# Kernel optimization log

Measured on AMD Instinct MI355X. Metric: run time of the kernel, lower is better.

Reference implementation:

```python
import jax, jax.numpy as jnp
import numpy as np

H = 768
NHEADS = 2
MAX_REL = 96  # module's max_rel_enc; static here (positive count >> 96 for these inputs)


def _ln(x, g, b, eps=1e-5):
    m = jnp.mean(x, axis=-1, keepdims=True)
    v = jnp.var(x, axis=-1, keepdims=True)
    return (x - m) * jax.lax.rsqrt(v + eps) * g + b


def _mha(q, k, v, in_w, in_b, out_w, out_b, key_pad):
    # q [B,Lq,H], k/v [B,Lk,H], key_pad [B,Lk] bool (True = masked key)
    d = q.shape[-1]
    dh = d // NHEADS
    wq, wk, wv = jnp.split(in_w, 3, axis=0)
    bq, bk, bv = jnp.split(in_b, 3)
    qh = (q @ wq.T + bq).reshape(q.shape[0], q.shape[1], NHEADS, dh)
    kh = (k @ wk.T + bk).reshape(k.shape[0], k.shape[1], NHEADS, dh)
    vh = (v @ wv.T + bv).reshape(v.shape[0], v.shape[1], NHEADS, dh)
    scores = jnp.einsum('bqhd,bkhd->bhqk', qh, kh) / np.float32(np.sqrt(dh))
    scores = jnp.where(key_pad[:, None, None, :], jnp.float32(-1e9), scores)
    attn = jax.nn.softmax(scores, axis=-1)
    out = jnp.einsum('bhqk,bkhd->bqhd', attn, vh).reshape(q.shape)
    return out @ out_w.T + out_b


def _forward(hidden_states, logits_prev, block_mask, W_rel, b_rel,
             enc_in_w, enc_in_b, enc_out_w, enc_out_b,
             enc_l1_w, enc_l1_b, enc_l2_w, enc_l2_b,
             enc_ln1_g, enc_ln1_b, enc_ln2_g, enc_ln2_b,
             dec_in_w, dec_in_b, dec_out_w, dec_out_b,
             dec_l1_w, dec_l1_b, dec_l2_w, dec_l2_b,
             dec_ln1_g, dec_ln1_b, dec_ln2_g, dec_ln2_b,
             fc_w, fc_b):
    B, N, Hd = hidden_states.shape
    # rel_layer(cat([h_i, h_j])) == h_i @ Wa.T + h_j @ Wb.T + b  (avoids [B,N,N,2H] intermediate)
    Wa = W_rel[:, :Hd]
    Wb = W_rel[:, Hd:]
    A = hidden_states @ Wa.T   # [B,N,H]
    C = hidden_states @ Wb.T   # [B,N,H]
    feat_pair = (A[:, :, None, :] + C[:, None, :, :] + b_rel).reshape(B, N * N, Hd)

    bm = block_mask.astype(jnp.float32)
    pair_mask = (bm[:, :, None] * bm[:, None, :]).reshape(B, N * N)
    score = jax.nn.sigmoid(logits_prev).reshape(B, N * N)
    neg = (score < 0.5).astype(jnp.float32)
    neg = 1.0 - (1.0 - neg) * pair_mask           # 1 = negative-or-invalid pair
    neg = jax.lax.stop_gradient(neg)              # matches score_prev.detach_()

    # dynamic top-k gather of positive pairs (static MAX_REL here)
    idx = jnp.argsort(neg, axis=1)[:, :MAX_REL]                     # positives (neg==0) first
    enc_pad = jnp.take_along_axis(neg, idx, axis=1) > 0.5           # [B,MAX_REL]
    enc_pad = enc_pad.at[:, 0].set(False)
    feat_now = feat_pair * (1.0 - neg)[:, :, None]
    pos_pairs = jnp.take_along_axis(feat_now, idx[:, :, None], axis=1)  # [B,MAX_REL,H]

    # 1-layer transformer encoder (post-norm, ReLU, d_ff = H)
    x = pos_pairs
    x = _ln(x + _mha(x, x, x, enc_in_w, enc_in_b, enc_out_w, enc_out_b, enc_pad),
            enc_ln1_g, enc_ln1_b)
    ff = jax.nn.relu(x @ enc_l1_w.T + enc_l1_b) @ enc_l2_w.T + enc_l2_b
    patterns = _ln(x + ff, enc_ln2_g, enc_ln2_b)

    # 1-layer decoder with self_attn=False: cross-attn + FFN, post-norm
    t = feat_pair
    t = _ln(t + _mha(t, patterns, patterns, dec_in_w, dec_in_b, dec_out_w, dec_out_b, enc_pad),
            dec_ln1_g, dec_ln1_b)
    ff = jax.nn.relu(t @ dec_l1_w.T + dec_l1_b) @ dec_l2_w.T + dec_l2_b
    t = _ln(t + ff, dec_ln2_g, dec_ln2_b)

    refined = t.reshape(B, N, N, Hd)
    return (refined @ fc_w.T + fc_b)[..., 0]    # [B,N,N]


def setup_inputs() -> dict:
    key = jax.random.key(0)
    ks = jax.random.split(key, 24)
    B, N = 4, 128
    p = lambda k, s: jax.random.normal(k, s, jnp.float32) * 0.02
    return {
        'hidden_states': jax.random.normal(ks[0], (B, N, H), jnp.float32),
        'logits_prev': jax.random.normal(ks[1], (B, N, N), jnp.float32),
        'block_mask': jax.random.randint(ks[2], (B, N), 0, 2),
        'W_rel': p(ks[3], (H, 2 * H)), 'b_rel': p(ks[4], (H,)),
        'enc_in_w': p(ks[5], (3 * H, H)), 'enc_in_b': p(ks[6], (3 * H,)),
        'enc_out_w': p(ks[7], (H, H)), 'enc_out_b': p(ks[8], (H,)),
        'enc_l1_w': p(ks[9], (H, H)), 'enc_l1_b': p(ks[10], (H,)),
        'enc_l2_w': p(ks[11], (H, H)), 'enc_l2_b': p(ks[12], (H,)),
        'enc_ln1_g': jnp.ones((H,), jnp.float32), 'enc_ln1_b': jnp.zeros((H,), jnp.float32),
        'enc_ln2_g': jnp.ones((H,), jnp.float32), 'enc_ln2_b': jnp.zeros((H,), jnp.float32),
        'dec_in_w': p(ks[13], (3 * H, H)), 'dec_in_b': p(ks[14], (3 * H,)),
        'dec_out_w': p(ks[15], (H, H)), 'dec_out_b': p(ks[16], (H,)),
        'dec_l1_w': p(ks[17], (H, H)), 'dec_l1_b': p(ks[18], (H,)),
        'dec_l2_w': p(ks[19], (H, H)), 'dec_l2_b': p(ks[20], (H,)),
        'dec_ln1_g': jnp.ones((H,), jnp.float32), 'dec_ln1_b': jnp.zeros((H,), jnp.float32),
        'dec_ln2_g': jnp.ones((H,), jnp.float32), 'dec_ln2_b': jnp.zeros((H,), jnp.float32),
        'fc_w': p(ks[21], (1, H)), 'fc_b': p(ks[22], (1,)),
    }


def reference(hidden_states, logits_prev, block_mask, W_rel, b_rel,
              enc_in_w, enc_in_b, enc_out_w, enc_out_b,
              enc_l1_w, enc_l1_b, enc_l2_w, enc_l2_b,
              enc_ln1_g, enc_ln1_b, enc_ln2_g, enc_ln2_b,
              dec_in_w, dec_in_b, dec_out_w, dec_out_b,
              dec_l1_w, dec_l1_b, dec_l2_w, dec_l2_b,
              dec_ln1_g, dec_ln1_b, dec_ln2_g, dec_ln2_b,
              fc_w, fc_b):
    return _forward(hidden_states, logits_prev, block_mask, W_rel, b_rel,
                    enc_in_w, enc_in_b, enc_out_w, enc_out_b,
                    enc_l1_w, enc_l1_b, enc_l2_w, enc_l2_b,
                    enc_ln1_g, enc_ln1_b, enc_ln2_g, enc_ln2_b,
                    dec_in_w, dec_in_b, dec_out_w, dec_out_b,
                    dec_l1_w, dec_l1_b, dec_l2_w, dec_l2_b,
                    dec_ln1_g, dec_ln1_b, dec_ln2_g, dec_ln2_b,
                    fc_w, fc_b)
```

## Files before the change

kernel.cpp:

```cpp
#include <hip/hip_runtime.h>
#include <cstdint>
#include <cstddef>

typedef unsigned short u16;
typedef __attribute__((ext_vector_type(8))) short sv8;
typedef __attribute__((ext_vector_type(4))) short sv4;
typedef __attribute__((ext_vector_type(4))) float fv4;
typedef __attribute__((ext_vector_type(8))) __bf16 bv8;

#define WAITVM(N) asm volatile("s_waitcnt vmcnt(" #N ")" ::: "memory")
#define WAITLG(N) asm volatile("s_waitcnt lgkmcnt(" #N ")" ::: "memory")
#define SB0() __builtin_amdgcn_sched_barrier(0)
#define BAR() __builtin_amdgcn_s_barrier()

__device__ __forceinline__ float b2f(u16 u) {
  union { unsigned int i; float f; } v; v.i = ((unsigned int)u) << 16; return v.f;
}
__device__ __forceinline__ u16 f2b(float f) {
  union { float f; unsigned int i; } v; v.f = f;
  unsigned int r = v.i + 0x7fffu + ((v.i >> 16) & 1u);
  return (u16)(r >> 16);
}

__device__ __forceinline__ void gload16(const u16* g, u16* l) {
  __builtin_amdgcn_global_load_lds(
      (const __attribute__((address_space(1))) void*)g,
      (__attribute__((address_space(3))) void*)l, 16, 0, 0);
}

struct CvtArgs { const float* src[10]; u16* dst[10]; int n[10]; };

__global__ __launch_bounds__(256) void cvt_multi(CvtArgs a) {
  int t = blockIdx.y;
  const float* s = a.src[t];
  u16* d = a.dst[t];
  int n = a.n[t];
  int i4 = (blockIdx.x * 256 + threadIdx.x) * 4;
  if (i4 + 4 <= n) {
    float4 v = *(const float4*)(s + i4);
    sv4 o;
    o[0] = (short)f2b(v.x); o[1] = (short)f2b(v.y);
    o[2] = (short)f2b(v.z); o[3] = (short)f2b(v.w);
    *(sv4*)(d + i4) = o;
  }
}

__global__ __launch_bounds__(256) void prep_q0(
    const float* __restrict__ dec_in_w, const float* __restrict__ dec_in_b,
    const float* __restrict__ b_rel, float* __restrict__ q0) {
  int wave = threadIdx.x >> 6, lane = threadIdx.x & 63;
  int row = blockIdx.x * 4 + wave;
  const float* wrp = dec_in_w + (size_t)row * 768;
  float acc = 0.f;
  #pragma unroll
  for (int t = 0; t < 3; t++) {
    float4 wv = *(const float4*)(wrp + (t * 64 + lane) * 4);
    float4 bv = *(const float4*)(b_rel + (t * 64 + lane) * 4);
    acc += wv.x * bv.x + wv.y * bv.y + wv.z * bv.z + wv.w * bv.w;
  }
  #pragma unroll
  for (int d = 1; d <= 32; d <<= 1) acc += __shfl_xor(acc, d);
  if (lane == 0) q0[row] = acc + dec_in_b[row];
}

__global__ __launch_bounds__(256) void prep_q0k(
    const float* __restrict__ q0, const u16* __restrict__ khb,
    float* __restrict__ q0k) {
  int wave = threadIdx.x >> 6, lane = threadIdx.x & 63;
  int idx = blockIdx.x * 4 + wave;
  int b = idx / 192, c = idx % 192;
  int h = (c < 96) ? 0 : 1;
  int k = (c < 96) ? c : c - 96;
  const u16* kr = khb + ((size_t)(b * 96 + k)) * 768 + h * 384;
  const float* qp = q0 + h * 384;
  float acc = 0.f;
  #pragma unroll
  for (int t = 0; t < 6; t++) {
    int d = t * 64 + lane;
    acc += qp[d] * b2f(kr[d]);
  }
  #pragma unroll
  for (int d = 1; d <= 32; d <<= 1) acc += __shfl_xor(acc, d);
  if (lane == 0) q0k[idx] = acc * 0.05103103630798287f;
}

__global__ __launch_bounds__(256) void prep_misc(
    const float* __restrict__ dec_out_b, const float* __restrict__ b_rel,
    const float* __restrict__ ln2g, const float* __restrict__ ln2b,
    const float* __restrict__ fc_w, const float* __restrict__ fc_b,
    float* __restrict__ bb, float* __restrict__ gfc, float* __restrict__ scal) {
  int tid = threadIdx.x;
  int wave = tid >> 6, lane = tid & 63;
  float s1 = 0.f, s2 = 0.f;
  for (int t = tid; t < 768; t += 256) {
    bb[t] = dec_out_b[t] + b_rel[t];
    float gf = ln2g[t] * fc_w[t];
    gfc[t] = gf;
    s1 += gf; s2 += ln2b[t] * fc_w[t];
  }
  #pragma unroll
  for (int d = 1; d <= 32; d <<= 1) { s1 += __shfl_xor(s1, d); s2 += __shfl_xor(s2, d); }
  __shared__ float r1[4], r2[4];
  if (lane == 0) { r1[wave] = s1; r2[wave] = s2; }
  __syncthreads();
  if (tid == 0) {
    float a = r1[0] + r1[1] + r1[2] + r1[3];
    float c = r2[0] + r2[1] + r2[2] + r2[3];
    scal[1] = a;
    scal[0] = c + fc_b[0];
  }
}

__global__ __launch_bounds__(256) void select_pairs(
    const float* __restrict__ logits, const int* __restrict__ bm,
    int* __restrict__ idxb, int* __restrict__ encpad, int* __restrict__ zflag) {
  int b = blockIdx.x, tid = threadIdx.x;
  int wave = tid >> 6, lane = tid & 63;
  __shared__ unsigned char pos[16384];
  __shared__ int bml[128];
  __shared__ int wsum[4];
  const float* lg = logits + (size_t)b * 16384;
  if (tid < 128) bml[tid] = bm[b * 128 + tid];
  __syncthreads();
  for (int i = 0; i < 16; i++) {
    int e4 = (i * 256 + tid) * 4;
    float4 v = *(const float4*)(lg + e4);
    uchar4 o;
    {
      float sg = 1.f / (1.f + expf(-v.x));
      o.x = (!(sg < 0.5f)) && bml[e4 >> 7] && bml[e4 & 127];
      sg = 1.f / (1.f + expf(-v.y));
      o.y = (!(sg < 0.5f)) && bml[(e4 + 1) >> 7] && bml[(e4 + 1) & 127];
      sg = 1.f / (1.f + expf(-v.z));
      o.z = (!(sg < 0.5f)) && bml[(e4 + 2) >> 7] && bml[(e4 + 2) & 127];
      sg = 1.f / (1.f + expf(-v.w));
      o.w = (!(sg < 0.5f)) && bml[(e4 + 3) >> 7] && bml[(e4 + 3) & 127];
    }
    *(uchar4*)(pos + e4) = o;
  }
  __syncthreads();
  int cnt = 0;
  #pragma unroll 8
  for (int u = 0; u < 64; u++) cnt += pos[tid * 64 + u];
  int v = cnt;
  #pragma unroll
  for (int d = 1; d < 64; d <<= 1) { int o = __shfl_up(v, d); if (lane >= d) v += o; }
  if (lane == 63) wsum[wave] = v;
  __syncthreads();
  int wbase = 0;
  for (int w = 0; w < wave; w++) wbase += wsum[w];
  int mtot = wsum[0] + wsum[1] + wsum[2] + wsum[3];
  int pq = wbase + v - cnt;
  int nq = tid * 64 - pq;
  for (int u = 0; u < 64; u++) {
    int p = tid * 64 + u;
    if (pos[p]) {
      if (pq < 96) { idxb[b * 96 + pq] = p; encpad[b * 96 + pq] = 0; zflag[b * 96 + pq] = 0; }
      pq++;
    } else {
      int slot = mtot + nq;
      if (slot < 96) { idxb[b * 96 + slot] = p; encpad[b * 96 + slot] = 1; zflag[b * 96 + slot] = 1; }
      nq++;
    }
  }
  __syncthreads();
  if (tid == 0) encpad[b * 96] = 0;
}

__global__ __launch_bounds__(256) void gather_pp(
    const float* __restrict__ Af, const float* __restrict__ Cf,
    const float* __restrict__ b_rel, const int* __restrict__ idxb,
    const int* __restrict__ zflag, u16* __restrict__ PP) {
  int s = blockIdx.x, b = blockIdx.y;
  int slot = b * 96 + s;
  int p = idxb[slot];
  int z = zflag[slot];
  const float* ar = Af + ((size_t)b * 128 + (p >> 7)) * 768;
  const float* cr = Cf + ((size_t)b * 128 + (p & 127)) * 768;
  for (int c = threadIdx.x; c < 768; c += 256) {
    float v = z ? 0.f : (ar[c] + cr[c] + b_rel[c]);
    PP[(size_t)slot * 768 + c] = f2b(v);
  }
}

template<int EPI, int OUTM, int BM>
__global__ __launch_bounds__(256) void gemm_bt(
    const u16* __restrict__ Aptr, const u16* __restrict__ Wptr,
    const float* __restrict__ bias,
    void* __restrict__ out1, void* __restrict__ out2,
    const u16* __restrict__ resp, int ldr,
    int M, int N, int K, int lda, int ldw, int ldo,
    int ZH, int zbm, int bstr,
    long sAb, long sAh, long sWb, long sWh, long sOb, long sOh,
    float scale) {
  constexpr int FR = BM / 32;
  constexpr int BUF = BM * 32;
  int z = blockIdx.z;
  int zb = z / ZH, zh = z % ZH;
  const u16* A = Aptr + (size_t)zb * sAb + (size_t)zh * sAh;
  const u16* W = Wptr + (size_t)(zb & zbm) * sWb + (size_t)zh * sWh;
  const float* bz = bias ? bias + (size_t)zb * bstr : nullptr;
  size_t obase = (size_t)zb * sOb + (size_t)zh * sOh;

  int m0 = blockIdx.x * BM, n0 = blockIdx.y * BM;
  int tid = threadIdx.x;
  int wave = tid >> 6, lane = tid & 63;
  int wr = (wave >> 1) * (BM / 2), wc = (wave & 1) * (BM / 2);

  __shared__ __attribute__((aligned(16))) u16 As[4 * BUF];
  __shared__ __attribute__((aligned(16))) u16 Ws[4 * BUF];

  fv4 acc[FR][FR] = {};

  int srow = tid & (BM - 1);
  int scol = (BM == 128) ? ((tid >> 7) * 8) : ((tid >> 6) * 8);
  int ra = m0 + srow; if (ra > M - 1) ra = M - 1;
  int rw = n0 + srow; if (rw > N - 1) rw = N - 1;
  const u16* gA = A + (size_t)ra * lda + scol;
  const u16* gW = W + (size_t)rw * ldw + scol;
  int lofs = wave * 512;

  int rb = (lane >> 4) * (BM * 8) + (lane & 15) * 8;

  int nt = K >> 5;

  auto stage = [&](int tile) {
    int k0 = tile << 5;
    int cu = tile & 3;
    u16* la = As + cu * BUF + lofs;
    u16* lw = Ws + cu * BUF + lofs;
    gload16(gA + k0, la);
    gload16(gW + k0, lw);
    if (BM == 128) {
      gload16(gA + k0 + 16, la + 2048);
      gload16(gW + k0 + 16, lw + 2048);
    }
  };

  auto compute = [&](int cu) {
    const u16* Ap = As + cu * BUF;
    const u16* Wp = Ws + cu * BUF;
    bv8 af[FR], wf[FR];
    #pragma unroll
    for (int f = 0; f < FR; f++) af[f] = *(const bv8*)(Ap + rb + (wr + f * 16) * 8);
    #pragma unroll
    for (int f = 0; f < FR; f++) wf[f] = *(const bv8*)(Wp + rb + (wc + f * 16) * 8);
    __builtin_amdgcn_s_setprio(1);
    #pragma unroll
    for (int fm = 0; fm < FR; fm++)
      #pragma unroll
      for (int fn = 0; fn < FR; fn++)
        acc[fm][fn] = __builtin_amdgcn_mfma_f32_16x16x32_bf16(af[fm], wf[fn], acc[fm][fn], 0, 0, 0);
    __builtin_amdgcn_s_setprio(0);
  };

  stage(0); stage(1); stage(2);

  for (int t = 0; t < nt - 3; ++t) {
    if constexpr (BM == 128) WAITVM(8); else WAITVM(4);
    BAR();
    stage(t + 3);
    SB0();
    compute(t & 3);
  }
  { if constexpr (BM == 128) WAITVM(8); else WAITVM(4); BAR(); SB0(); compute((nt - 3) & 3); }
  { if constexpr (BM == 128) WAITVM(4); else WAITVM(2); BAR(); SB0(); compute((nt - 2) & 3); }
  { WAITVM(0); BAR(); SB0(); compute((nt - 1) & 3); }

  int lr4 = (lane >> 4) * 4, lc = lane & 15;
  #pragma unroll
  for (int fm = 0; fm < FR; fm++) {
    #pragma unroll
    for (int r = 0; r < 4; r++) {
      int row = m0 + wr + fm * 16 + lr4 + r;
      if (row >= M) continue;
      #pragma unroll
      for (int fn = 0; fn < FR; fn++) {
        int col = n0 + wc + fn * 16 + lc;
        if (col >= N) continue;
        float v = acc[fm][fn][r] * scale;
        if (bz) v += bz[col];
        if (EPI == 1) v = fmaxf(v, 0.f);
        if (EPI == 2) v += b2f(resp[(size_t)row * ldr + col]);
        size_t o = obase + (size_t)row * ldo + col;
        if (OUTM == 0) ((u16*)out1)[o] = f2b(v);
        else if (OUTM == 1) ((float*)out1)[o] = v;
        else { ((float*)out1)[o] = v; ((u16*)out2)[o] = f2b(v); }
      }
    }
  }
}

template<int EPI>
__global__ __launch_bounds__(512, 2) void gemm256(
    const u16* __restrict__ Aptr, const u16* __restrict__ Wptr,
    const float* __restrict__ bias, u16* __restrict__ out,
    const u16* __restrict__ resp, int ldr,
    const u16* __restrict__ exA, const u16* __restrict__ exC,
    int K, int lda, int ldw, int ldo,
    long zA, long zW, long zO, long zR, long zE) {
  __shared__ __attribute__((aligned(16))) u16 lds[2 * 2 * 16384];

  int nzz = gridDim.z;
  int lin = blockIdx.x + 64 * (blockIdx.y + 3 * blockIdx.z);
  int xcd = lin & 7;
  int s = lin >> 3;
  int grp = s / (3 * nzz);
  int rem = s - grp * (3 * nzz);
  int by = rem / nzz;
  int zz = rem - by * nzz;
  int bx = xcd + 8 * grp;

  const u16* A = Aptr + (size_t)zz * zA;
  const u16* W = Wptr + (size_t)zz * zW;
  u16* outz = out + (size_t)zz * zO;
  const u16* respz = resp + (size_t)zz * zR;
  const u16* exAz = exA + (size_t)zz * zE;
  const u16* exCz = exC + (size_t)zz * zE;

  int m0 = bx * 256, n0 = by * 256;
  int tid = threadIdx.x;
  int wave = tid >> 6, lane = tid & 63;
  int wr = (wave >> 2) * 128;
  int wc = (wave & 3) * 64;
  int lr = lane & 15, ls = lane >> 4;
  int axor = lr & 7;

  int srow = tid >> 3;
  int schunk = (tid & 7) ^ (srow & 7);
  const u16* gA0 = A + (size_t)(m0 + srow) * lda + schunk * 8;
  const u16* gW0 = W + (size_t)(n0 + srow) * ldw + schunk * 8;
  int wofs = wave * 512;

  fv4 acc[8][4] = {};

  auto stageA = [&](int t, int q) {
    gload16(gA0 + (size_t)q * 64 * lda + t * 64,
            lds + (t & 1) * 32768 + q * 4096 + wofs);
  };
  auto stageW = [&](int t, int q) {
    gload16(gW0 + (size_t)q * 64 * ldw + t * 64,
            lds + (t & 1) * 32768 + 16384 + q * 4096 + wofs);
  };

  int TH = K >> 6;
  #pragma unroll
  for (int q = 0; q < 4; q++) stageA(0, q);
  #pragma unroll
  for (int q = 0; q < 4; q++) stageW(0, q);
  WAITVM(0);
  BAR();

  int k0o = (ls ^ axor) * 8;
  int k1o = ((ls + 4) ^ axor) * 8;

  for (int t = 0; t < TH; ++t) {
    const u16* Ab = lds + (t & 1) * 32768;
    const u16* Wb = Ab + 16384;
    bool st = (t + 1 < TH);
    bv8 af[4], wf[4];
    #pragma unroll
    for (int n = 0; n < 4; n++)
      wf[n] = *(const bv8*)(Wb + (wc + n * 16 + lr) * 64 + k0o);
    #pragma unroll
    for (int f = 0; f < 4; f++)
      af[f] = *(const bv8*)(Ab + (wr + f * 16 + lr) * 64 + k0o);
    if (st) { stageA(t + 1, 0); stageA(t + 1, 1); stageA(t + 1, 2); stageA(t + 1, 3); }
    WAITLG(0); SB0();
    __builtin_amdgcn_s_setprio(1);
    #pragma unroll
    for (int f = 0; f < 4; f++)
      #pragma unroll
      for (int n = 0; n < 4; n++)
        acc[f][n] = __builtin_amdgcn_mfma_f32_16x16x32_bf16(af[f], wf[n], acc[f][n], 0, 0, 0);
    __builtin_amdgcn_s_setprio(0);
    #pragma unroll
    for (int f = 0; f < 4; f++)
      af[f] = *(const bv8*)(Ab + (wr + 64 + f * 16 + lr) * 64 + k0o);
    if (st) { stageW(t + 1, 0); stageW(t + 1, 1); stageW(t + 1, 2); stageW(t + 1, 3); }
    WAITLG(0); SB0();
    __builtin_amdgcn_s_setprio(1);
    #pragma unroll
    for (int f = 0; f < 4; f++)
      #pragma unroll
      for (int n = 0; n < 4; n++)
        acc[4 + f][n] = __builtin_amdgcn_mfma_f32_16x16x32_bf16(af[f], wf[n], acc[4 + f][n], 0, 0, 0);
    __builtin_amdgcn_s_setprio(0);
    #pragma unroll
    for (int n = 0; n < 4; n++)
      wf[n] = *(const bv8*)(Wb + (wc + n * 16 + lr) * 64 + k1o);
    #pragma unroll
    for (int f = 0; f < 4; f++)
      af[f] = *(const bv8*)(Ab + (wr + f * 16 + lr) * 64 + k1o);
    WAITLG(0); SB0();
    __builtin_amdgcn_s_setprio(1);
    #pragma unroll
    for (int f = 0; f < 4; f++)
      #pragma unroll
      for (int n = 0; n < 4; n++)
        acc[f][n] = __builtin_amdgcn_mfma_f32_16x16x32_bf16(af[f], wf[n], acc[f][n], 0, 0, 0);
    __builtin_amdgcn_s_setprio(0);
    #pragma unroll
    for (int f = 0; f < 4; f++)
      af[f] = *(const bv8*)(Ab + (wr + 64 + f * 16 + lr) * 64 + k1o);
    WAITLG(0); SB0();
    __builtin_amdgcn_s_setprio(1);
    #pragma unroll
    for (int f = 0; f < 4; f++)
      #pragma unroll
      for (int n = 0; n < 4; n++)
        acc[4 + f][n] = __builtin_amdgcn_mfma_f32_16x16x32_bf16(af[f], wf[n], acc[4 + f][n], 0, 0, 0);
    __builtin_amdgcn_s_setprio(0);
    if (st) WAITVM(0);
    BAR();
  }

  if (EPI == 3) {
    for (int c = tid; c < 4096; c += 512) {
      int rrow = c >> 5, c8 = c & 31;
      *(sv8*)(lds + (size_t)c * 8) =
          *(const sv8*)(exCz + (size_t)rrow * 768 + n0 + c8 * 8);
    }
    if (tid < 64) {
      int rrow = tid >> 5, c8 = tid & 31;
      *(sv8*)(lds + 32768 + (size_t)tid * 8) =
          *(const sv8*)(exAz + (size_t)(bx * 2 + rrow) * 768 + n0 + c8 * 8);
    }
    __syncthreads();
  }

  int lr4 = (lane >> 4) * 4, lc = lane & 15;
  #pragma unroll
  for (int fm = 0; fm < 8; fm++) {
    #pragma unroll
    for (int r = 0; r < 4; r++) {
      int row = m0 + wr + (fm >> 2) * 64 + (fm & 3) * 16 + lr4 + r;
      #pragma unroll
      for (int fn = 0; fn < 4; fn++) {
        int col = n0 + wc + fn * 16 + lc;
        float v = acc[fm][fn][r] + bias[col];
        if (EPI == 1) v = fmaxf(v, 0.f);
        if (EPI == 2) v += b2f(respz[(size_t)row * ldr + col]);
        if (EPI == 3) v += b2f(lds[32768 + (size_t)((row - m0) >> 7) * 256 + (col - n0)])
                         + b2f(lds[(size_t)(row & 127) * 256 + (col - n0)]);
        outz[(size_t)row * ldo + col] = f2b(v);
      }
    }
  }
}

__global__ __launch_bounds__(128) void enc_att(
    const u16* __restrict__ QKV, const int* __restrict__ encpad, u16* __restrict__ AO) {
  int s = blockIdx.x;
  int bh = blockIdx.y;
  int b = bh >> 1, h = bh & 1;
  int tid = threadIdx.x;
  __shared__ float q[384];
  __shared__ float sc[96];
  __shared__ float red[2];
  size_t rowq = ((size_t)b * 96 + s) * 2304;
  for (int d = tid; d < 384; d += 128) q[d] = b2f(QKV[rowq + h * 384 + d]);
  __syncthreads();
  if (tid < 96) {
    const u16* kr = QKV + ((size_t)b * 96 + tid) * 2304 + 768 + h * 384;
    float acc = 0.f;
    for (int d = 0; d < 384; d++) acc += q[d] * b2f(kr[d]);
    acc *= 0.05103103630798287f;
    if (encpad[b * 96 + tid]) acc = -1e9f;
    sc[tid] = acc;
  }
  __syncthreads();
  if (tid == 0) {
    float m = sc[0];
    for (int k = 1; k < 96; k++) m = fmaxf(m, sc[k]);
    red[0] = m;
  }
  __syncthreads();
  if (tid < 96) sc[tid] = __expf(sc[tid] - red[0]);
  __syncthreads();
  if (tid == 0) {
    float sum = 0.f;
    for (int k = 0; k < 96; k++) sum += sc[k];
    red[1] = 1.f / sum;
  }
  __syncthreads();
  float inv = red[1];
  for (int d = tid; d < 384; d += 128) {
    const u16* vb = QKV + (size_t)b * 96 * 2304 + 1536 + h * 384 + d;
    float acc = 0.f;
    for (int k = 0; k < 96; k++) acc += sc[k] * b2f(vb[(size_t)k * 2304]);
    AO[((size_t)b * 96 + s) * 768 + h * 384 + d] = f2b(acc * inv);
  }
}

__global__ __launch_bounds__(256) void softmax_pairs(
    const float* __restrict__ SA, const float* __restrict__ SC,
    const float* __restrict__ q0k,
    const int* __restrict__ encpad, u16* __restrict__ P) {
  int wave = threadIdx.x >> 6, lane = threadIdx.x & 63;
  int bi = blockIdx.y;
  int p = blockIdx.x * 4 + wave;
  int i = p >> 7, j = p & 127;
  const float* sa = SA + ((size_t)bi * 128 + i) * 192;
  const float* sc = SC + ((size_t)bi * 128 + j) * 192;
  const float* qk = q0k + bi * 192;
  int c0 = lane * 3;
  float s0, s1, s2;
  {
    int c = c0;     int k = (c < 96) ? c : c - 96;
    s0 = encpad[bi * 96 + k] ? -1e9f : (sa[c] + sc[c] + qk[c]);
    c = c0 + 1;     k = (c < 96) ? c : c - 96;
    s1 = encpad[bi * 96 + k] ? -1e9f : (sa[c] + sc[c] + qk[c]);
    c = c0 + 2;     k = (c < 96) ? c : c - 96;
    s2 = encpad[bi * 96 + k] ? -1e9f : (sa[c] + sc[c] + qk[c]);
  }
  float m = fmaxf(s0, fmaxf(s1, s2));
  #pragma unroll
  for (int d = 1; d <= 16; d <<= 1) m = fmaxf(m, __shfl_xor(m, d));
  float e0 = __expf(s0 - m), e1 = __expf(s1 - m), e2 = __expf(s2 - m);
  float sum = e0 + e1 + e2;
  #pragma unroll
  for (int d = 1; d <= 16; d <<= 1) sum += __shfl_xor(sum, d);
  float inv = 1.f / sum;
  u16* o = P + ((size_t)bi * 16384 + p) * 192 + c0;
  o[0] = f2b(e0 * inv); o[1] = f2b(e1 * inv); o[2] = f2b(e2 * inv);
}

__global__ __launch_bounds__(256) void ln_rows(
    const u16* __restrict__ Y, const float* __restrict__ g,
    const float* __restrict__ bt, u16* __restrict__ X, int rows) {
  int wave = threadIdx.x >> 6, lane = threadIdx.x & 63;
  int row = blockIdx.x * 4 + wave;
  if (row >= rows) return;
  const u16* y = Y + (size_t)row * 768;
  sv8 v1 = *(const sv8*)(y + lane * 8);
  sv4 v2 = *(const sv4*)(y + 512 + lane * 4);
  float x[12];
  #pragma unroll
  for (int t = 0; t < 8; t++) x[t] = b2f((u16)v1[t]);
  #pragma unroll
  for (int t = 0; t < 4; t++) x[8 + t] = b2f((u16)v2[t]);
  float s = 0.f, q = 0.f;
  #pragma unroll
  for (int t = 0; t < 12; t++) { s += x[t]; q += x[t] * x[t]; }
  #pragma unroll
  for (int d = 1; d <= 32; d <<= 1) { s += __shfl_xor(s, d); q += __shfl_xor(q, d); }
  float mean = s * (1.f / 768.f);
  float var = q * (1.f / 768.f) - mean * mean;
  float rstd = rsqrtf(var + 1e-5f);
  u16* xo = X + (size_t)row * 768;
  sv8 w1; sv4 w2;
  #pragma unroll
  for (int t = 0; t < 8; t++) {
    int c = lane * 8 + t;
    w1[t] = (short)f2b((x[t] - mean) * rstd * g[c] + bt[c]);
  }
  #pragma unroll
  for (int t = 0; t < 4; t++) {
    int c = 512 + lane * 4 + t;
    w2[t] = (short)f2b((x[8 + t] - mean) * rstd * g[c] + bt[c]);
  }
  *(sv8*)(xo + lane * 8) = w1;
  *(sv4*)(xo + 512 + lane * 4) = w2;
}

__global__ __launch_bounds__(256) void final_rows(
    const u16* __restrict__ Y, const float* __restrict__ gfc,
    const float* __restrict__ scal, float* __restrict__ out, int rows) {
  int wave = threadIdx.x >> 6, lane = threadIdx.x & 63;
  int row = blockIdx.x * 4 + wave;
  if (row >= rows) return;
  const u16* y = Y + (size_t)row * 768;
  sv8 v1 = *(const sv8*)(y + lane * 8);
  sv4 v2 = *(const sv4*)(y + 512 + lane * 4);
  float x[12];
  #pragma unroll
  for (int t = 0; t < 8; t++) x[t] = b2f((u16)v1[t]);
  #pragma unroll
  for (int t = 0; t < 4; t++) x[8 + t] = b2f((u16)v2[t]);
  float s = 0.f, q = 0.f, sg = 0.f;
  #pragma unroll
  for (int t = 0; t < 8; t++) {
    int c = lane * 8 + t;
    s += x[t]; q += x[t] * x[t]; sg += x[t] * gfc[c];
  }
  #pragma unroll
  for (int t = 0; t < 4; t++) {
    int c = 512 + lane * 4 + t;
    s += x[8 + t]; q += x[8 + t] * x[8 + t]; sg += x[8 + t] * gfc[c];
  }
  #pragma unroll
  for (int d = 1; d <= 32; d <<= 1) {
    s += __shfl_xor(s, d); q += __shfl_xor(q, d); sg += __shfl_xor(sg, d);
  }
  float mean = s * (1.f / 768.f);
  float var = q * (1.f / 768.f) - mean * mean;
  float rstd = rsqrtf(var + 1e-5f);
  if (lane == 0) out[row] = rstd * (sg - mean * scal[1]) + scal[0];
}

extern "C" void kernel_launch(void* const* d_in, const int* in_sizes, int n_in,
                              void* d_out, int out_size, void* d_ws, size_t ws_size,
                              hipStream_t stream) {
  (void)in_sizes; (void)n_in; (void)out_size;
  const float* hs        = (const float*)d_in[0];
  const float* logits    = (const float*)d_in[1];
  const int*   bmask     = (const int*)d_in[2];
  const float* W_rel     = (const float*)d_in[3];
  const float* b_rel     = (const float*)d_in[4];
  const float* enc_in_w  = (const float*)d_in[5];
  const float* enc_in_b  = (const float*)d_in[6];
  const float* enc_out_w = (const float*)d_in[7];
  const float* enc_out_b = (const float*)d_in[8];
  const float* enc_l1_w  = (const float*)d_in[9];
  const float* enc_l1_b  = (const float*)d_in[10];
  const float* enc_l2_w  = (const float*)d_in[11];
  const float* enc_l2_b  = (const float*)d_in[12];
  const float* enc_ln1_g = (const float*)d_in[13];
  const float* enc_ln1_b = (const float*)d_in[14];
  const float* enc_ln2_g = (const float*)d_in[15];
  const float* enc_ln2_b = (const float*)d_in[16];
  const float* dec_in_w  = (const float*)d_in[17];
  const float* dec_in_b  = (const float*)d_in[18];
  const float* dec_out_w = (const float*)d_in[19];
  const float* dec_out_b = (const float*)d_in[20];
  const float* dec_l1_w  = (const float*)d_in[21];
  const float* dec_l1_b  = (const float*)d_in[22];
  const float* dec_l2_w  = (const float*)d_in[23];
  const float* dec_l2_b  = (const float*)d_in[24];
  const float* dec_ln1_g = (const float*)d_in[25];
  const float* dec_ln1_b = (const float*)d_in[26];
  const float* dec_ln2_g = (const float*)d_in[27];
  const float* dec_ln2_b = (const float*)d_in[28];
  const float* fc_w      = (const float*)d_in[29];
  const float* fc_b      = (const float*)d_in[30];

  char* base = (char*)d_ws;
  size_t off = 0;
  auto alloc = [&](size_t bytes) -> void* {
    size_t o = (off + 255) & ~(size_t)255;
    off = o + bytes;
    return (void*)(base + o);
  };

  u16* hsb   = (u16*)alloc((size_t)393216 * 2);
  u16* wrelb = (u16*)alloc((size_t)1179648 * 2);
  u16* eiwb  = (u16*)alloc((size_t)1769472 * 2);
  u16* eowb  = (u16*)alloc((size_t)589824 * 2);
  u16* el1b  = (u16*)alloc((size_t)589824 * 2);
  u16* el2b  = (u16*)alloc((size_t)589824 * 2);
  u16* diwb  = (u16*)alloc((size_t)1769472 * 2);
  u16* dowb  = (u16*)alloc((size_t)589824 * 2);
  u16* dl1b  = (u16*)alloc((size_t)589824 * 2);
  u16* dl2b  = (u16*)alloc((size_t)589824 * 2);
  float* Af  = (float*)alloc((size_t)786432 * 4);
  float* Cf  = Af + 393216;
  u16* ACb   = (u16*)alloc((size_t)786432 * 2);
  float* q0  = (float*)alloc(768 * 4);
  float* q0k = (float*)alloc(768 * 4);
  float* bbv = (float*)alloc(768 * 4);
  float* gfc = (float*)alloc(768 * 4);
  float* scal = (float*)alloc(4 * 4);
  int* idxb   = (int*)alloc(384 * 4);
  int* encpadb = (int*)alloc(384 * 4);
  int* zflagb  = (int*)alloc(384 * 4);
  u16* PPb   = (u16*)alloc((size_t)294912 * 2);
  u16* QKVe  = (u16*)alloc((size_t)884736 * 2);
  u16* AOe   = (u16*)alloc((size_t)294912 * 2);
  u16* Ye    = (u16*)alloc((size_t)294912 * 2);
  u16* Xe    = (u16*)alloc((size_t)294912 * 2);
  u16* He    = (u16*)alloc((size_t)294912 * 2);
  u16* Y2e   = (u16*)alloc((size_t)294912 * 2);
  u16* patternsb = (u16*)alloc((size_t)294912 * 2);
  u16* khb   = (u16*)alloc((size_t)294912 * 2);
  u16* vhb   = (u16*)alloc((size_t)294912 * 2);
  u16* AqCqb = (u16*)alloc((size_t)786432 * 2);
  float* SASCf = (float*)alloc((size_t)196608 * 4);
  u16* VOTb  = (u16*)alloc((size_t)589824 * 2);
  u16* Pb    = (u16*)alloc((size_t)12582912 * 2);

  const size_t ACT1 = (size_t)12582912 * 2;
  size_t fixed = (off + 255) & ~(size_t)255;
  int NB = 1;
  if (fixed + 2 * 4 * ACT1 + 4096 <= ws_size) NB = 4;
  else if (fixed + 2 * 2 * ACT1 + 4096 <= ws_size) NB = 2;
  u16* Y1buf = (u16*)alloc((size_t)NB * 12582912 * 2);
  u16* H1buf = (u16*)alloc((size_t)NB * 12582912 * 2);

  CvtArgs ca{};
  int ci = 0;
  auto addc = [&](const float* s, u16* d, int n) { ca.src[ci] = s; ca.dst[ci] = d; ca.n[ci] = n; ci++; };
  addc(hs, hsb, 393216);        addc(W_rel, wrelb, 1179648);
  addc(enc_in_w, eiwb, 1769472); addc(enc_out_w, eowb, 589824);
  addc(enc_l1_w, el1b, 589824);  addc(enc_l2_w, el2b, 589824);
  addc(dec_in_w, diwb, 1769472); addc(dec_out_w, dowb, 589824);
  addc(dec_l1_w, dl1b, 589824);  addc(dec_l2_w, dl2b, 589824);
  cvt_multi<<<dim3(1728, 10, 1), 256, 0, stream>>>(ca);

  prep_q0<<<192, 256, 0, stream>>>(dec_in_w, dec_in_b, b_rel, q0);
  prep_misc<<<1, 256, 0, stream>>>(dec_out_b, b_rel, dec_ln2_g, dec_ln2_b, fc_w, fc_b,
                                   bbv, gfc, scal);
  select_pairs<<<dim3(4, 1, 1), 256, 0, stream>>>(logits, bmask, idxb, encpadb, zflagb);

  gemm_bt<0, 2, 64><<<dim3(8, 12, 2), 256, 0, stream>>>(hsb, wrelb, nullptr, Af, ACb,
      nullptr, 0, 512, 768, 768, 768, 1536, 768,
      1, -1, 0, 0, 0, 768, 0, 393216, 0, 1.f);

  gather_pp<<<dim3(96, 4, 1), 256, 0, stream>>>(Af, Cf, b_rel, idxb, zflagb, PPb);

  gemm_bt<0, 0, 64><<<dim3(6, 36, 1), 256, 0, stream>>>(PPb, eiwb, enc_in_b, QKVe, nullptr,
      nullptr, 0, 384, 2304, 768, 768, 768, 2304,
      1, -1, 0, 0, 0, 0, 0, 0, 0, 1.f);
  enc_att<<<dim3(96, 8, 1), 128, 0, stream>>>(QKVe, encpadb, AOe);
  gemm_bt<2, 0, 64><<<dim3(6, 12, 1), 256, 0, stream>>>(AOe, eowb, enc_out_b, Ye, nullptr,
      PPb, 768, 384, 768, 768, 768, 768, 768,
      1, -1, 0, 0, 0, 0, 0, 0, 0, 1.f);
  ln_rows<<<96, 256, 0, stream>>>(Ye, enc_ln1_g, enc_ln1_b, Xe, 384);
  gemm_bt<1, 0, 64><<<dim3(6, 12, 1), 256, 0, stream>>>(Xe, el1b, enc_l1_b, He, nullptr,
      nullptr, 0, 384, 768, 768, 768, 768, 768,
      1, -1, 0, 0, 0, 0, 0, 0, 0, 1.f);
  gemm_bt<2, 0, 64><<<dim3(6, 12, 1), 256, 0, stream>>>(He, el2b, enc_l2_b, Y2e, nullptr,
      Xe, 768, 384, 768, 768, 768, 768, 768,
      1, -1, 0, 0, 0, 0, 0, 0, 0, 1.f);
  ln_rows<<<96, 256, 0, stream>>>(Y2e, enc_ln2_g, enc_ln2_b, patternsb, 384);

  gemm_bt<0, 0, 64><<<dim3(6, 12, 2), 256, 0, stream>>>(patternsb, diwb + (size_t)768 * 768,
      dec_in_b + 768, khb, nullptr, nullptr, 0,
      384, 768, 768, 768, 768, 768,
      1, -1, 768, 0, 0, 589824, 0, 294912, 0, 1.f);
  prep_q0k<<<192, 256, 0, stream>>>(q0, khb, q0k);
  gemm_bt<0, 0, 64><<<dim3(16, 12, 1), 256, 0, stream>>>(ACb, diwb, nullptr, AqCqb, nullptr,
      nullptr, 0, 1024, 768, 768, 768, 768, 768,
      1, -1, 0, 0, 0, 0, 0, 0, 0, 1.f);
  const float scl = 0.05103103630798287f;
  gemm_bt<0, 1, 64><<<dim3(2, 2, 16), 256, 0, stream>>>(AqCqb, khb, nullptr, SASCf, nullptr,
      nullptr, 0, 128, 96, 384, 768, 768, 192,
      2, 3, 0, 98304, 384, 73728, 384, 24576, 96, scl);
  gemm_bt<0, 0, 64><<<dim3(12, 2, 8), 256, 0, stream>>>(dowb, vhb, nullptr, VOTb, nullptr,
      nullptr, 0, 768, 96, 384, 768, 768, 192,
      2, -1, 0, 0, 384, 73728, 384, 147456, 96, 1.f);

  softmax_pairs<<<dim3(4096, 4), 256, 0, stream>>>(SASCf, SASCf + 98304, q0k, encpadb, Pb);
  const long PB_B = 3145728, VOT_B = 147456, ACT_B = 12582912;
  const long EXU_B = 98304;
  for (int g = 0; g < 4; g += NB) {
    gemm256<3><<<dim3(64, 3, NB), 512, 0, stream>>>(
        Pb + (size_t)g * PB_B, VOTb + (size_t)g * VOT_B, bbv, Y1buf,
        Y1buf, 0,
        ACb + (size_t)g * EXU_B,
        ACb + 393216 + (size_t)g * EXU_B,
        192, 192, 192, 768, PB_B, VOT_B, ACT_B, 0, EXU_B);
    ln_rows<<<NB * 4096, 256, 0, stream>>>(Y1buf, dec_ln1_g, dec_ln1_b, Y1buf, NB * 16384);
    gemm256<1><<<dim3(64, 3, NB), 512, 0, stream>>>(
        Y1buf, dl1b, dec_l1_b, H1buf, H1buf, 0, ACb, ACb,
        768, 768, 768, 768, ACT_B, 0, ACT_B, 0, 0);
    gemm256<2><<<dim3(64, 3, NB), 512, 0, stream>>>(
        H1buf, dl2b, dec_l2_b, Y1buf, Y1buf, 768, ACb, ACb,
        768, 768, 768, 768, ACT_B, 0, ACT_B, ACT_B, 0);
    final_rows<<<NB * 4096, 256, 0, stream>>>(Y1buf, gfc, scal,
        (float*)d_out + (size_t)g * 16384, NB * 16384);
  }
}
```

Measured before the change: 505.0 us.

## Fold decoder LayerNorms into GEMM epilogues via atomic row statistics

```diff
diff --git a/kernel.cpp b/kernel.cpp
--- a/kernel.cpp
+++ b/kernel.cpp
@@ -45,22 +45,69 @@
   }
 }
 
-__global__ __launch_bounds__(256) void prep_q0(
+__global__ __launch_bounds__(256) void cvt_scale(
+    const float* __restrict__ s, const float* __restrict__ g, u16* __restrict__ d) {
+  int i4 = (blockIdx.x * 256 + threadIdx.x) * 4;
+  if (i4 + 4 <= 589824) {
+    float4 v = *(const float4*)(s + i4);
+    int k = i4 % 768;
+    sv4 o;
+    o[0] = (short)f2b(v.x * g[k]);
+    o[1] = (short)f2b(v.y * g[k + 1]);
+    o[2] = (short)f2b(v.z * g[k + 2]);
+    o[3] = (short)f2b(v.w * g[k + 3]);
+    *(sv4*)(d + i4) = o;
+  }
+}
+
+__global__ __launch_bounds__(256) void prep_mv(
     const float* __restrict__ dec_in_w, const float* __restrict__ dec_in_b,
-    const float* __restrict__ b_rel, float* __restrict__ q0) {
-  int wave = threadIdx.x >> 6, lane = threadIdx.x & 63;
-  int row = blockIdx.x * 4 + wave;
-  const float* wrp = dec_in_w + (size_t)row * 768;
-  float acc = 0.f;
-  #pragma unroll
-  for (int t = 0; t < 3; t++) {
-    float4 wv = *(const float4*)(wrp + (t * 64 + lane) * 4);
-    float4 bv = *(const float4*)(b_rel + (t * 64 + lane) * 4);
-    acc += wv.x * bv.x + wv.y * bv.y + wv.z * bv.z + wv.w * bv.w;
-  }
-  #pragma unroll
-  for (int d = 1; d <= 32; d <<= 1) acc += __shfl_xor(acc, d);
-  if (lane == 0) q0[row] = acc + dec_in_b[row];
+    const float* __restrict__ b_rel, float* __restrict__ q0,
+    const float* __restrict__ l1w, const float* __restrict__ l1b,
+    const float* __restrict__ ln1g, const float* __restrict__ ln1b,
+    float* __restrict__ b1p, float* __restrict__ cs1,
+    const float* __restrict__ dec_out_b,
+    const float* __restrict__ ln2g, const float* __restrict__ ln2b,
+    const float* __restrict__ fc_w, const float* __restrict__ fc_b,
+    float* __restrict__ bb, float* __restrict__ gfc, float* __restrict__ scal) {
+  int blk = blockIdx.x;
+  int tid = threadIdx.x, wave = tid >> 6, lane = tid & 63;
+  if (blk < 576) {
+    const float* wsrc; const float* vsrc; float* dst; const float* badd;
+    int base;
+    if (blk < 192)      { wsrc = dec_in_w; vsrc = b_rel; dst = q0;  badd = dec_in_b; base = blk; }
+    else if (blk < 384) { wsrc = l1w;      vsrc = ln1b;  dst = b1p; badd = l1b;      base = blk - 192; }
+    else                { wsrc = l1w;      vsrc = ln1g;  dst = cs1; badd = nullptr;  base = blk - 384; }
+    int row = base * 4 + wave;
+    const float* wrp = wsrc + (size_t)row * 768;
+    float acc = 0.f;
+    #pragma unroll
+    for (int t = 0; t < 3; t++) {
+      float4 wv = *(const float4*)(wrp + (t * 64 + lane) * 4);
+      float4 bv = *(const float4*)(vsrc + (t * 64 + lane) * 4);
+      acc += wv.x * bv.x + wv.y * bv.y + wv.z * bv.z + wv.w * bv.w;
+    }
+    #pragma unroll
+    for (int d = 1; d <= 32; d <<= 1) acc += __shfl_xor(acc, d);
+    if (lane == 0) dst[row] = acc + (badd ? badd[row] : 0.f);
+  } else {
+    float s1 = 0.f, s2 = 0.f;
+    for (int t = tid; t < 768; t += 256) {
+      bb[t] = dec_out_b[t] + b_rel[t];
+      float gf = ln2g[t] * fc_w[t];
+      gfc[t] = gf;
+      s1 += gf; s2 += ln2b[t] * fc_w[t];
+    }
+    #pragma unroll
+    for (int d = 1; d <= 32; d <<= 1) { s1 += __shfl_xor(s1, d); s2 += __shfl_xor(s2, d); }
+    __shared__ float r1[4], r2[4];
+    if (lane == 0) { r1[wave] = s1; r2[wave] = s2; }
+    __syncthreads();
+    if (tid == 0) {
+      scal[1] = r1[0] + r1[1] + r1[2] + r1[3];
+      scal[0] = r2[0] + r2[1] + r2[2] + r2[3] + fc_b[0];
+    }
+  }
 }
 
 __global__ __launch_bounds__(256) void prep_q0k(
@@ -82,33 +129,6 @@
   #pragma unroll
   for (int d = 1; d <= 32; d <<= 1) acc += __shfl_xor(acc, d);
   if (lane == 0) q0k[idx] = acc * 0.05103103630798287f;
-}
-
-__global__ __launch_bounds__(256) void prep_misc(
-    const float* __restrict__ dec_out_b, const float* __restrict__ b_rel,
-    const float* __restrict__ ln2g, const float* __restrict__ ln2b,
-    const float* __restrict__ fc_w, const float* __restrict__ fc_b,
-    float* __restrict__ bb, float* __restrict__ gfc, float* __restrict__ scal) {
-  int tid = threadIdx.x;
-  int wave = tid >> 6, lane = tid & 63;
-  float s1 = 0.f, s2 = 0.f;
-  for (int t = tid; t < 768; t += 256) {
-    bb[t] = dec_out_b[t] + b_rel[t];
-    float gf = ln2g[t] * fc_w[t];
-    gfc[t] = gf;
-    s1 += gf; s2 += ln2b[t] * fc_w[t];
-  }
-  #pragma unroll
-  for (int d = 1; d <= 32; d <<= 1) { s1 += __shfl_xor(s1, d); s2 += __shfl_xor(s2, d); }
-  __shared__ float r1[4], r2[4];
-  if (lane == 0) { r1[wave] = s1; r2[wave] = s2; }
-  __syncthreads();
-  if (tid == 0) {
-    float a = r1[0] + r1[1] + r1[2] + r1[3];
-    float c = r2[0] + r2[1] + r2[2] + r2[3];
-    scal[1] = a;
-    scal[0] = c + fc_b[0];
-  }
 }
 
 __global__ __launch_bounds__(256) void select_pairs(
@@ -297,6 +317,9 @@
     const float* __restrict__ bias, u16* __restrict__ out,
     const u16* __restrict__ resp, int ldr,
     const u16* __restrict__ exA, const u16* __restrict__ exC,
+    const float* __restrict__ stA, float* __restrict__ stO,
+    const float* __restrict__ vA, const float* __restrict__ vB,
+    const float* __restrict__ vC,
     int K, int lda, int ldw, int ldo,
     long zA, long zW, long zO, long zR, long zE) {
   __shared__ __attribute__((aligned(16))) u16 lds[2 * 2 * 16384];
@@ -317,6 +340,7 @@
   const u16* respz = resp + (size_t)zz * zR;
   const u16* exAz = exA + (size_t)zz * zE;
   const u16* exCz = exC + (size_t)zz * zE;
+  size_t zrow = (size_t)zz * 16384;
 
   int m0 = bx * 256, n0 = by * 256;
   int tid = threadIdx.x;
@@ -435,15 +459,51 @@
     #pragma unroll
     for (int r = 0; r < 4; r++) {
       int row = m0 + wr + (fm >> 2) * 64 + (fm & 3) * 16 + lr4 + r;
+      float mu = 0.f, rr = 0.f;
+      if (EPI == 4 || EPI == 5) {
+        float s1v = stA[(zrow + row) * 2];
+        float q1v = stA[(zrow + row) * 2 + 1];
+        mu = s1v * (1.f / 768.f);
+        rr = rsqrtf(q1v * (1.f / 768.f) - mu * mu + 1e-5f);
+      }
+      float sv = 0.f, qv = 0.f, gv = 0.f;
       #pragma unroll
       for (int fn = 0; fn < 4; fn++) {
         int col = n0 + wc + fn * 16 + lc;
-        float v = acc[fm][fn][r] + bias[col];
-        if (EPI == 1) v = fmaxf(v, 0.f);
-        if (EPI == 2) v += b2f(respz[(size_t)row * ldr + col]);
-        if (EPI == 3) v += b2f(lds[32768 + (size_t)((row - m0) >> 7) * 256 + (col - n0)])
-                         + b2f(lds[(size_t)(row & 127) * 256 + (col - n0)]);
-        outz[(size_t)row * ldo + col] = f2b(v);
+        float a = acc[fm][fn][r];
+        if (EPI == 3) {
+          float v = a + bias[col]
+                  + b2f(lds[32768 + (size_t)((row - m0) >> 7) * 256 + (col - n0)])
+                  + b2f(lds[(size_t)(row & 127) * 256 + (col - n0)]);
+          outz[(size_t)row * ldo + col] = f2b(v);
+          sv += v; qv += v * v;
+        } else if (EPI == 4) {
+          float v = rr * (a - mu * vA[col]) + bias[col];
+          v = fmaxf(v, 0.f);
+          outz[(size_t)row * ldo + col] = f2b(v);
+        } else {
+          float xres = (b2f(respz[(size_t)row * ldr + col]) - mu) * rr * vA[col] + vB[col];
+          float v = a + bias[col] + xres;
+          sv += v; qv += v * v; gv += vC[col] * v;
+        }
+      }
+      if (EPI == 3 || EPI == 5) {
+        #pragma unroll
+        for (int d = 1; d <= 8; d <<= 1) {
+          sv += __shfl_xor(sv, d);
+          qv += __shfl_xor(qv, d);
+          if (EPI == 5) gv += __shfl_xor(gv, d);
+        }
+        if (lc == 0) {
+          if (EPI == 3) {
+            atomicAdd(&stO[(zrow + row) * 2], sv);
+            atomicAdd(&stO[(zrow + row) * 2 + 1], qv);
+          } else {
+            atomicAdd(&stO[(zrow + row) * 3], sv);
+            atomicAdd(&stO[(zrow + row) * 3 + 1], qv);
+            atomicAdd(&stO[(zrow + row) * 3 + 2], gv);
+          }
+        }
       }
     }
   }
@@ -564,39 +624,18 @@
   *(sv4*)(xo + 512 + lane * 4) = w2;
 }
 
-__global__ __launch_bounds__(256) void final_rows(
-    const u16* __restrict__ Y, const float* __restrict__ gfc,
-    const float* __restrict__ scal, float* __restrict__ out, int rows) {
-  int wave = threadIdx.x >> 6, lane = threadIdx.x & 63;
-  int row = blockIdx.x * 4 + wave;
+__global__ __launch_bounds__(256) void finish_rows(
+    const float* __restrict__ st2, const float* __restrict__ scal,
+    float* __restrict__ out, int rows) {
+  int row = blockIdx.x * 256 + threadIdx.x;
   if (row >= rows) return;
-  const u16* y = Y + (size_t)row * 768;
-  sv8 v1 = *(const sv8*)(y + lane * 8);
-  sv4 v2 = *(const sv4*)(y + 512 + lane * 4);
-  float x[12];
-  #pragma unroll
-  for (int t = 0; t < 8; t++) x[t] = b2f((u16)v1[t]);
-  #pragma unroll
-  for (int t = 0; t < 4; t++) x[8 + t] = b2f((u16)v2[t]);
-  float s = 0.f, q = 0.f, sg = 0.f;
-  #pragma unroll
-  for (int t = 0; t < 8; t++) {
-    int c = lane * 8 + t;
-    s += x[t]; q += x[t] * x[t]; sg += x[t] * gfc[c];
-  }
-  #pragma unroll
-  for (int t = 0; t < 4; t++) {
-    int c = 512 + lane * 4 + t;
-    s += x[8 + t]; q += x[8 + t] * x[8 + t]; sg += x[8 + t] * gfc[c];
-  }
-  #pragma unroll
-  for (int d = 1; d <= 32; d <<= 1) {
-    s += __shfl_xor(s, d); q += __shfl_xor(q, d); sg += __shfl_xor(sg, d);
-  }
+  float s = st2[(size_t)row * 3];
+  float q = st2[(size_t)row * 3 + 1];
+  float sg = st2[(size_t)row * 3 + 2];
   float mean = s * (1.f / 768.f);
   float var = q * (1.f / 768.f) - mean * mean;
   float rstd = rsqrtf(var + 1e-5f);
-  if (lane == 0) out[row] = rstd * (sg - mean * scal[1]) + scal[0];
+  out[row] = rstd * (sg - mean * scal[1]) + scal[0];
 }
 
 extern "C" void kernel_launch(void* const* d_in, const int* in_sizes, int n_in,
@@ -660,6 +699,8 @@
   float* q0k = (float*)alloc(768 * 4);
   float* bbv = (float*)alloc(768 * 4);
   float* gfc = (float*)alloc(768 * 4);
+  float* b1p = (float*)alloc(768 * 4);
+  float* cs1 = (float*)alloc(768 * 4);
   float* scal = (float*)alloc(4 * 4);
   int* idxb   = (int*)alloc(384 * 4);
   int* encpadb = (int*)alloc(384 * 4);
@@ -677,6 +718,9 @@
   u16* AqCqb = (u16*)alloc((size_t)786432 * 2);
   float* SASCf = (float*)alloc((size_t)196608 * 4);
   u16* VOTb  = (u16*)alloc((size_t)589824 * 2);
+  float* stats1 = (float*)alloc((size_t)65536 * 2 * 4);
+  float* stats2 = (float*)alloc((size_t)65536 * 3 * 4);
+  size_t statsBytes = (size_t)((char*)(stats2 + 65536 * 3) - (char*)stats1);
   u16* Pb    = (u16*)alloc((size_t)12582912 * 2);
 
   const size_t ACT1 = (size_t)12582912 * 2;
@@ -694,12 +738,14 @@
   addc(enc_in_w, eiwb, 1769472); addc(enc_out_w, eowb, 589824);
   addc(enc_l1_w, el1b, 589824);  addc(enc_l2_w, el2b, 589824);
   addc(dec_in_w, diwb, 1769472); addc(dec_out_w, dowb, 589824);
-  addc(dec_l1_w, dl1b, 589824);  addc(dec_l2_w, dl2b, 589824);
+  addc(dec_l2_w, dl2b, 589824);
+  ca.src[9] = nullptr; ca.dst[9] = nullptr; ca.n[9] = 0;
   cvt_multi<<<dim3(1728, 10, 1), 256, 0, stream>>>(ca);
-
-  prep_q0<<<192, 256, 0, stream>>>(dec_in_w, dec_in_b, b_rel, q0);
-  prep_misc<<<1, 256, 0, stream>>>(dec_out_b, b_rel, dec_ln2_g, dec_ln2_b, fc_w, fc_b,
-                                   bbv, gfc, scal);
+  cvt_scale<<<576, 256, 0, stream>>>(dec_l1_w, dec_ln1_g, dl1b);
+
+  prep_mv<<<577, 256, 0, stream>>>(dec_in_w, dec_in_b, b_rel, q0,
+      dec_l1_w, dec_l1_b, dec_ln1_g, dec_ln1_b, b1p, cs1,
+      dec_out_b, dec_ln2_g, dec_ln2_b, fc_w, fc_b, bbv, gfc, scal);
   select_pairs<<<dim3(4, 1, 1), 256, 0, stream>>>(logits, bmask, idxb, encpadb, zflagb);
 
   gemm_bt<0, 2, 64><<<dim3(8, 12, 2), 256, 0, stream>>>(hsb, wrelb, nullptr, Af, ACb,
@@ -741,6 +787,8 @@
       2, -1, 0, 0, 384, 73728, 384, 147456, 96, 1.f);
 
   softmax_pairs<<<dim3(4096, 4), 256, 0, stream>>>(SASCf, SASCf + 98304, q0k, encpadb, Pb);
+  hipMemsetAsync(stats1, 0, statsBytes, stream);
+
   const long PB_B = 3145728, VOT_B = 147456, ACT_B = 12582912;
   const long EXU_B = 98304;
   for (int g = 0; g < 4; g += NB) {
@@ -749,15 +797,21 @@
         Y1buf, 0,
         ACb + (size_t)g * EXU_B,
         ACb + 393216 + (size_t)g * EXU_B,
+        nullptr, stats1 + (size_t)g * 16384 * 2,
+        nullptr, nullptr, nullptr,
         192, 192, 192, 768, PB_B, VOT_B, ACT_B, 0, EXU_B);
-    ln_rows<<<NB * 4096, 256, 0, stream>>>(Y1buf, dec_ln1_g, dec_ln1_b, Y1buf, NB * 16384);
-    gemm256<1><<<dim3(64, 3, NB), 512, 0, stream>>>(
-        Y1buf, dl1b, dec_l1_b, H1buf, H1buf, 0, ACb, ACb,
+    gemm256<4><<<dim3(64, 3, NB), 512, 0, stream>>>(
+        Y1buf, dl1b, b1p, H1buf,
+        H1buf, 0, ACb, ACb,
+        stats1 + (size_t)g * 16384 * 2, nullptr,
+        cs1, nullptr, nullptr,
         768, 768, 768, 768, ACT_B, 0, ACT_B, 0, 0);
-    gemm256<2><<<dim3(64, 3, NB), 512, 0, stream>>>(
-        H1buf, dl2b, dec_l2_b, Y1buf, Y1buf, 768, ACb, ACb,
+    gemm256<5><<<dim3(64, 3, NB), 512, 0, stream>>>(
+        H1buf, dl2b, dec_l2_b, Y1buf,
+        Y1buf, 768, ACb, ACb,
+        stats1 + (size_t)g * 16384 * 2, stats2 + (size_t)g * 16384 * 3,
+        dec_ln1_g, dec_ln1_b, gfc,
         768, 768, 768, 768, ACT_B, 0, ACT_B, ACT_B, 0);
-    final_rows<<<NB * 4096, 256, 0, stream>>>(Y1buf, gfc, scal,
-        (float*)d_out + (size_t)g * 16384, NB * 16384);
-  }
-}
+  }
+  finish_rows<<<256, 256, 0, stream>>>(stats2, scal, (float*)d_out, 65536);
+}
```

Result: slower. 667.4 us (+32.2%).
